# Kernel optimization log

Hardware: AMD Instinct MI355X
Metric: run time of the kernel (lower is better)

The kernel has to match this reference:

```python
import jax, jax.numpy as jnp
import numpy as np

D_MODEL = 1024
N_HEADS = 16
HEAD_DIM = D_MODEL // N_HEADS
D_FF = 4096
EPS = 1e-5


def setup_inputs() -> dict:
    key = jax.random.key(0)
    ks = jax.random.split(key, 12)
    s = 0.02
    return {
        "x": jax.random.normal(ks[0], (2, 2048, D_MODEL), jnp.float32),
        "wq": jax.random.normal(ks[1], (D_MODEL, D_MODEL), jnp.float32) * s,
        "bq": jnp.zeros((D_MODEL,), jnp.float32),
        "wk": jax.random.normal(ks[2], (D_MODEL, D_MODEL), jnp.float32) * s,
        "bk": jnp.zeros((D_MODEL,), jnp.float32),
        "wv": jax.random.normal(ks[3], (D_MODEL, D_MODEL), jnp.float32) * s,
        "bv": jnp.zeros((D_MODEL,), jnp.float32),
        "wo": jax.random.normal(ks[4], (D_MODEL, D_MODEL), jnp.float32) * s,
        "bo": jnp.zeros((D_MODEL,), jnp.float32),
        "w1": jax.random.normal(ks[5], (D_MODEL, D_FF), jnp.float32) * s,
        "b1": jnp.zeros((D_FF,), jnp.float32),
        "w2": jax.random.normal(ks[6], (D_FF, D_MODEL), jnp.float32) * s,
        "b2": jnp.zeros((D_MODEL,), jnp.float32),
        "g1": jnp.ones((D_MODEL,), jnp.float32),
        "be1": jnp.zeros((D_MODEL,), jnp.float32),
        "g2": jnp.ones((D_MODEL,), jnp.float32),
        "be2": jnp.zeros((D_MODEL,), jnp.float32),
    }


def _layer_norm(x, g, b):
    mu = jnp.mean(x, axis=-1, keepdims=True)
    var = jnp.var(x, axis=-1, keepdims=True)
    return (x - mu) * jax.lax.rsqrt(var + EPS) * g + b


def reference(x, wq, bq, wk, bk, wv, bv, wo, bo, w1, b1, w2, b2, g1, be1, g2, be2):
    B, S, D = x.shape
    nx = _layer_norm(x, g1, be1)
    # projections -> [B, H, S, d]
    def split_heads(t):
        return t.reshape(B, S, N_HEADS, HEAD_DIM).transpose(0, 2, 1, 3)
    q = split_heads(nx @ wq + bq)
    k = split_heads(nx @ wk + bk)
    v = split_heads(nx @ wv + bv)
    scores = jnp.einsum("bhqd,bhkd->bhqk", q, k) / jnp.sqrt(jnp.float32(HEAD_DIM))
    attn = jax.nn.softmax(scores, axis=-1)
    out = jnp.einsum("bhqk,bhkd->bhqd", attn, v)
    out = out.transpose(0, 2, 1, 3).reshape(B, S, D)
    x = x + (out @ wo + bo)
    nx = _layer_norm(x, g2, be2)
    ff = jax.nn.relu(nx @ w1 + b1) @ w2 + b2
    return x + ff
```

## Files before the change

### kernel.cpp

```cpp
#include <hip/hip_runtime.h>


typedef __attribute__((ext_vector_type(8))) unsigned short u16x8;
typedef __attribute__((ext_vector_type(4))) unsigned short u16x4;
typedef __attribute__((ext_vector_type(8))) __bf16 bf16x8;
typedef __attribute__((ext_vector_type(4))) float f32x4;
typedef __attribute__((ext_vector_type(4))) unsigned int u32x4;

#define C_SCALE 0.1803368801111f

static __device__ __forceinline__ unsigned short f2b(float f) {
    return __builtin_bit_cast(unsigned short, (__bf16)f);
}
static __device__ __forceinline__ float b2f(unsigned short h) {
    unsigned u = ((unsigned)h) << 16;
    float f;
    __builtin_memcpy(&f, &u, 4);
    return f;
}

static __device__ __forceinline__ void async_cp16(
    const unsigned short* g, unsigned short* l)
{
    __builtin_amdgcn_global_load_lds(
        (const __attribute__((address_space(1))) unsigned int*)g,
        (__attribute__((address_space(3))) unsigned int*)l,
        16, 0, 0);
}

__global__ __launch_bounds__(256) void transpose_all_k(
    const float* __restrict__ wq, const float* __restrict__ wk,
    const float* __restrict__ wv, const float* __restrict__ wo,
    const float* __restrict__ w1, const float* __restrict__ w2,
    unsigned short* __restrict__ wqkvT, unsigned short* __restrict__ woT,
    unsigned short* __restrict__ w1T, unsigned short* __restrict__ w2T)
{
    __shared__ unsigned short tile[32][33];
    const int ti = blockIdx.x;
    const float* in;
    unsigned short* out;
    int R, C, bi, bj;
    float sc = 1.0f;
    if (ti < 4096) {
        R = 1024; C = 1024;
        bi = (ti & 1023) >> 5; bj = ti & 31;
        int z = ti >> 10;
        in = (z == 0) ? wq : (z == 1) ? wk : (z == 2) ? wv : wo;
        out = (z < 3) ? wqkvT + (size_t)z * 1024 * 1024 : woT;
        if (z == 1) sc = C_SCALE;
    } else if (ti < 8192) {
        R = 1024; C = 4096;
        int l = ti - 4096;
        bi = l >> 7; bj = l & 127;
        in = w1; out = w1T;
    } else {
        R = 4096; C = 1024;
        int l = ti - 8192;
        bi = l >> 5; bj = l & 31;
        in = w2; out = w2T;
    }
    const int tx = threadIdx.x & 31, ty = threadIdx.x >> 5;
#pragma unroll
    for (int rr = 0; rr < 4; ++rr) {
        int r = ty + rr * 8;
        tile[r][tx] = f2b(in[(size_t)(bi * 32 + r) * C + bj * 32 + tx] * sc);
    }
    __syncthreads();
#pragma unroll
    for (int rr = 0; rr < 4; ++rr) {
        int r = ty + rr * 8;
        out[(size_t)(bj * 32 + r) * R + bi * 32 + tx] = tile[tx][r];
    }
}

__global__ __launch_bounds__(256) void concat3_k(
    const float* __restrict__ a, const float* __restrict__ b,
    const float* __restrict__ c, float* __restrict__ o)
{
    int t = blockIdx.x * 256 + threadIdx.x;
    float v = (t < 1024) ? a[t]
            : ((t < 2048) ? b[t - 1024] * C_SCALE : c[t - 2048]);
    o[t] = v;
}

__global__ __launch_bounds__(256) void ln_kernel(
    const float* __restrict__ x, const float* __restrict__ g,
    const float* __restrict__ be, unsigned short* __restrict__ o)
{
    const int row = blockIdx.x;
    const int t = threadIdx.x;
    const float* xr = x + (size_t)row * 1024;
    float4 v4 = *reinterpret_cast<const float4*>(&xr[t * 4]);
    float f[4] = {v4.x, v4.y, v4.z, v4.w};
    float s = f[0] + f[1] + f[2] + f[3];
    float ss = f[0] * f[0] + f[1] * f[1] + f[2] * f[2] + f[3] * f[3];
#pragma unroll
    for (int d = 1; d < 64; d <<= 1) {
        s += __shfl_xor(s, d);
        ss += __shfl_xor(ss, d);
    }
    __shared__ float sb[4], ssb[4];
    const int wave = t >> 6;
    if ((t & 63) == 0) { sb[wave] = s; ssb[wave] = ss; }
    __syncthreads();
    s = sb[0] + sb[1] + sb[2] + sb[3];
    ss = ssb[0] + ssb[1] + ssb[2] + ssb[3];
    const float mu = s * (1.0f / 1024.0f);
    const float var = ss * (1.0f / 1024.0f) - mu * mu;
    const float rs = rsqrtf(var + 1e-5f);
    u16x4 r4;
#pragma unroll
    for (int j = 0; j < 4; ++j)
        r4[j] = f2b((f[j] - mu) * rs * g[t * 4 + j] + be[t * 4 + j]);
    *reinterpret_cast<u16x4*>(&o[(size_t)row * 1024 + t * 4]) = r4;
}

__global__ __launch_bounds__(256) void reduce_ln_kernel(
    const unsigned short* __restrict__ pa, const unsigned short* __restrict__ pb,
    const float* __restrict__ bias, const float* __restrict__ x,
    const float* __restrict__ g, const float* __restrict__ be,
    float* __restrict__ x2, unsigned short* __restrict__ o)
{
    const int row = blockIdx.x;
    const int t = threadIdx.x;
    const size_t base = (size_t)row * 1024 + t * 4;
    float4 x4 = *reinterpret_cast<const float4*>(&x[base]);
    float4 bb = *reinterpret_cast<const float4*>(&bias[t * 4]);
    float f[4] = {x4.x + bb.x, x4.y + bb.y, x4.z + bb.z, x4.w + bb.w};
#pragma unroll
    for (int z = 0; z < 2; ++z) {
        u16x4 va = *reinterpret_cast<const u16x4*>(&pa[(size_t)z * 4096 * 1024 + base]);
        u16x4 vb = *reinterpret_cast<const u16x4*>(&pb[(size_t)z * 4096 * 1024 + base]);
#pragma unroll
        for (int j = 0; j < 4; ++j) f[j] += b2f(va[j]) + b2f(vb[j]);
    }
    *reinterpret_cast<float4*>(&x2[base]) = {f[0], f[1], f[2], f[3]};
    float s = f[0] + f[1] + f[2] + f[3];
    float ss = f[0] * f[0] + f[1] * f[1] + f[2] * f[2] + f[3] * f[3];
#pragma unroll
    for (int d = 1; d < 64; d <<= 1) {
        s += __shfl_xor(s, d);
        ss += __shfl_xor(ss, d);
    }
    __shared__ float sb[4], ssb[4];
    const int wave = t >> 6;
    if ((t & 63) == 0) { sb[wave] = s; ssb[wave] = ss; }
    __syncthreads();
    s = sb[0] + sb[1] + sb[2] + sb[3];
    ss = ssb[0] + ssb[1] + ssb[2] + ssb[3];
    const float mu = s * (1.0f / 1024.0f);
    const float var = ss * (1.0f / 1024.0f) - mu * mu;
    const float rs = rsqrtf(var + 1e-5f);
    u16x4 r4;
#pragma unroll
    for (int j = 0; j < 4; ++j)
        r4[j] = f2b((f[j] - mu) * rs * g[t * 4 + j] + be[t * 4 + j]);
    *reinterpret_cast<u16x4*>(&o[base]) = r4;
}

__global__ __launch_bounds__(256) void reduce_out4_k(
    const unsigned short* __restrict__ pa, const unsigned short* __restrict__ pb,
    const float* __restrict__ bias, const float* __restrict__ x2,
    float* __restrict__ out)
{
    const size_t i4 = ((size_t)blockIdx.x * 256 + threadIdx.x) * 4;
    float4 x4 = *reinterpret_cast<const float4*>(&x2[i4]);
    float4 bb = *reinterpret_cast<const float4*>(&bias[i4 & 1023]);
    float a0 = x4.x + bb.x, a1 = x4.y + bb.y, a2 = x4.z + bb.z, a3 = x4.w + bb.w;
#pragma unroll
    for (int z = 0; z < 2; ++z) {
        u16x4 va = *reinterpret_cast<const u16x4*>(&pa[(size_t)z * 4096 * 1024 + i4]);
        u16x4 vb = *reinterpret_cast<const u16x4*>(&pb[(size_t)z * 4096 * 1024 + i4]);
        a0 += b2f(va[0]) + b2f(vb[0]);
        a1 += b2f(va[1]) + b2f(vb[1]);
        a2 += b2f(va[2]) + b2f(vb[2]);
        a3 += b2f(va[3]) + b2f(vb[3]);
    }
    *reinterpret_cast<float4*>(&out[i4]) = {a0, a1, a2, a3};
}

template<int MODE, int RELU>
__global__ __launch_bounds__(256, 4) void gemm_bt(
    const unsigned short* __restrict__ A, int lda,
    const unsigned short* __restrict__ Bt, int ldb,
    const float* __restrict__ bias,
    void* __restrict__ Cv, void* __restrict__ Cv2, int N, int Kloop)
{
    __shared__ unsigned short As[128 * 32];
    __shared__ unsigned short Bs[128 * 32];
    const int t = threadIdx.x;
    const int wave = t >> 6, lane = t & 63;
    const int quad = lane >> 4, l16 = lane & 15;
    const int wm = wave >> 1, wn = wave & 1;
    const int m0 = blockIdx.y * 128;
    const int n0 = blockIdx.x * 128;
    const int k0 = blockIdx.z * Kloop;
    const int rl = lane >> 2;
    const int cl = (lane & 3) * 8;

    f32x4 acc[4][4];
#pragma unroll
    for (int mi = 0; mi < 4; ++mi)
#pragma unroll
        for (int ni = 0; ni < 4; ++ni) acc[mi][ni] = {0.f, 0.f, 0.f, 0.f};

    for (int kt = 0; kt < Kloop; kt += 32) {
#pragma unroll
        for (int j = 0; j < 4; ++j) {
            int c = wave * 4 + j;
            if (c < 8) {
                async_cp16(&A[(size_t)(m0 + c * 16 + rl) * lda + k0 + kt + cl],
                           &As[c * 512 + lane * 8]);
            } else {
                int bc = c - 8;
                async_cp16(&Bt[(size_t)(n0 + bc * 16 + rl) * ldb + k0 + kt + cl],
                           &Bs[bc * 512 + lane * 8]);
            }
        }
        __syncthreads();
        bf16x8 af[4], bfr[4];
#pragma unroll
        for (int mi = 0; mi < 4; ++mi)
            af[mi] = __builtin_bit_cast(bf16x8,
                *reinterpret_cast<const u16x8*>(&As[(wm * 64 + mi * 16 + l16) * 32 + quad * 8]));
#pragma unroll
        for (int ni = 0; ni < 4; ++ni)
            bfr[ni] = __builtin_bit_cast(bf16x8,
                *reinterpret_cast<const u16x8*>(&Bs[(wn * 64 + ni * 16 + l16) * 32 + quad * 8]));
#pragma unroll
        for (int mi = 0; mi < 4; ++mi)
#pragma unroll
            for (int ni = 0; ni < 4; ++ni)
                acc[mi][ni] = __builtin_amdgcn_mfma_f32_16x16x32_bf16(
                    af[mi], bfr[ni], acc[mi][ni], 0, 0, 0);
        __syncthreads();
    }

#pragma unroll
    for (int mi = 0; mi < 4; ++mi) {
        const int gr0 = m0 + wm * 64 + mi * 16 + quad * 4;
#pragma unroll
        for (int ni = 0; ni < 4; ++ni) {
            const int gc = n0 + wn * 64 + ni * 16 + l16;
            if (MODE == 2) {
                const float bv = bias[gc];
                if (gc < 2048) {
#pragma unroll
                    for (int r = 0; r < 4; ++r)
                        ((unsigned short*)Cv)[(size_t)(gr0 + r) * 2048 + gc] =
                            f2b(acc[mi][ni][r] + bv);
                } else {
                    u16x4 pk;
#pragma unroll
                    for (int r = 0; r < 4; ++r) pk[r] = f2b(acc[mi][ni][r] + bv);
                    const int b = gr0 >> 11, s0 = gr0 & 2047;
                    *reinterpret_cast<u16x4*>(
                        &((unsigned short*)Cv2)[((size_t)b * 1024 + (gc - 2048)) * 2048 + s0]) = pk;
                }
            } else if (MODE == 5) {
                unsigned short* base = (blockIdx.z < 2)
                    ? (unsigned short*)Cv  + (size_t)blockIdx.z * 4096 * N
                    : (unsigned short*)Cv2 + (size_t)(blockIdx.z - 2) * 4096 * N;
#pragma unroll
                for (int r = 0; r < 4; ++r)
                    base[(size_t)(gr0 + r) * N + gc] = f2b(acc[mi][ni][r]);
            } else {
                const float bv = bias[gc];
#pragma unroll
                for (int r = 0; r < 4; ++r) {
                    float v = acc[mi][ni][r] + bv;
                    if (RELU) v = fmaxf(v, 0.f);
                    ((unsigned short*)Cv)[(size_t)(gr0 + r) * N + gc] = f2b(v);
                }
            }
        }
    }
}

__global__ __launch_bounds__(256, 2) void attn_kernel(
    const unsigned short* __restrict__ qkb, const unsigned short* __restrict__ vbT,
    unsigned short* __restrict__ ao)
{
    __shared__ unsigned short Ks[2][64][72];
    __shared__ unsigned short Vt[2][64][72];
    const int t = threadIdx.x;
    const int lane = t & 63;
    const int quad = lane >> 4, l16 = lane & 15;
    const int wave = t >> 6;
    const int bh = blockIdx.y;
    const int b = bh >> 4, h = bh & 15;
    const int q0 = blockIdx.x * 128 + wave * 32;
    const size_t qk_base = (size_t)b * 2048 * 2048;
    const size_t vt_base = (size_t)b * 1024 * 2048 + (size_t)h * 64 * 2048;

    bf16x8 qf[2][2];
#pragma unroll
    for (int m = 0; m < 2; ++m)
#pragma unroll
        for (int kk = 0; kk < 2; ++kk)
            qf[m][kk] = __builtin_bit_cast(bf16x8, *reinterpret_cast<const u16x8*>(
                &qkb[qk_base + (size_t)(q0 + m * 16 + l16) * 2048 + h * 64 + kk * 32 + quad * 8]));

    u16x8 ones_u;
#pragma unroll
    for (int j = 0; j < 8; ++j) ones_u[j] = 0x3F80;
    const bf16x8 onesf = __builtin_bit_cast(bf16x8, ones_u);

    f32x4 o_acc[2][4], l_frag[2];
#pragma unroll
    for (int m = 0; m < 2; ++m) {
        l_frag[m] = {0.f, 0.f, 0.f, 0.f};
#pragma unroll
        for (int nf = 0; nf < 4; ++nf) o_acc[m][nf] = {0.f, 0.f, 0.f, 0.f};
    }

    const int srow0 = t >> 3, sc8 = (t & 7) * 8;
    const int srow1 = srow0 + 32;

    const unsigned short* kg0 = &qkb[qk_base + (size_t)srow0 * 2048 + 1024 + h * 64 + sc8];
    const unsigned short* kg1 = kg0 + (size_t)32 * 2048;
    const unsigned short* vg0 = &vbT[vt_base + (size_t)srow0 * 2048 + sc8];
    const unsigned short* vg1 = vg0 + (size_t)32 * 2048;

    u16x8 kr[2], vr[2];
    kr[0] = *reinterpret_cast<const u16x8*>(kg0);
    kr[1] = *reinterpret_cast<const u16x8*>(kg1);
    vr[0] = *reinterpret_cast<const u16x8*>(vg0);
    vr[1] = *reinterpret_cast<const u16x8*>(vg1);
    *reinterpret_cast<u16x8*>(&Ks[0][srow0][sc8]) = kr[0];
    *reinterpret_cast<u16x8*>(&Ks[0][srow1][sc8]) = kr[1];
    *reinterpret_cast<u16x8*>(&Vt[0][srow0][sc8]) = vr[0];
    *reinterpret_cast<u16x8*>(&Vt[0][srow1][sc8]) = vr[1];
    kr[0] = *reinterpret_cast<const u16x8*>(kg0 + (size_t)64 * 2048);
    kr[1] = *reinterpret_cast<const u16x8*>(kg1 + (size_t)64 * 2048);
    vr[0] = *reinterpret_cast<const u16x8*>(vg0 + 64);
    vr[1] = *reinterpret_cast<const u16x8*>(vg1 + 64);
    __syncthreads();

    for (int it = 0; it < 32; ++it) {
        const int cur = it & 1, nxt = cur ^ 1;
        if (it + 1 < 32) {
            *reinterpret_cast<u16x8*>(&Ks[nxt][srow0][sc8]) = kr[0];
            *reinterpret_cast<u16x8*>(&Ks[nxt][srow1][sc8]) = kr[1];
            *reinterpret_cast<u16x8*>(&Vt[nxt][srow0][sc8]) = vr[0];
            *reinterpret_cast<u16x8*>(&Vt[nxt][srow1][sc8]) = vr[1];
        }
        if (it + 2 < 32) {
            const size_t ko = (size_t)(it + 2) * 64 * 2048;
            const int vo = (it + 2) * 64;
            kr[0] = *reinterpret_cast<const u16x8*>(kg0 + ko);
            kr[1] = *reinterpret_cast<const u16x8*>(kg1 + ko);
            vr[0] = *reinterpret_cast<const u16x8*>(vg0 + vo);
            vr[1] = *reinterpret_cast<const u16x8*>(vg1 + vo);
        }

#pragma unroll
        for (int kh = 0; kh < 2; ++kh) {
            unsigned d0[2][2], d1[2][2];
#pragma unroll
            for (int kfi = 0; kfi < 2; ++kfi) {
                const int kf = kh * 2 + kfi;
                bf16x8 kfr0 = __builtin_bit_cast(bf16x8,
                    *reinterpret_cast<const u16x8*>(&Ks[cur][kf * 16 + l16][quad * 8]));
                bf16x8 kfr1 = __builtin_bit_cast(bf16x8,
                    *reinterpret_cast<const u16x8*>(&Ks[cur][kf * 16 + l16][32 + quad * 8]));
#pragma unroll
                for (int m = 0; m < 2; ++m) {
                    f32x4 s = {0.f, 0.f, 0.f, 0.f};
                    s = __builtin_amdgcn_mfma_f32_16x16x32_bf16(kfr0, qf[m][0], s, 0, 0, 0);
                    s = __builtin_amdgcn_mfma_f32_16x16x32_bf16(kfr1, qf[m][1], s, 0, 0, 0);
                    d0[m][kfi] = (unsigned)f2b(exp2f(s[0])) |
                                 ((unsigned)f2b(exp2f(s[1])) << 16);
                    d1[m][kfi] = (unsigned)f2b(exp2f(s[2])) |
                                 ((unsigned)f2b(exp2f(s[3])) << 16);
                }
            }
            bf16x8 pfr[2];
#pragma unroll
            for (int m = 0; m < 2; ++m) {
                unsigned x0 = d0[m][0], y0 = d0[m][1];
                unsigned x1 = d1[m][0], y1 = d1[m][1];
                asm("v_permlane32_swap_b32 %0, %1\n\t"
                    "v_permlane16_swap_b32 %0, %1"
                    : "+v"(x0), "+v"(y0));
                asm("v_permlane32_swap_b32 %0, %1\n\t"
                    "v_permlane16_swap_b32 %0, %1"
                    : "+v"(x1), "+v"(y1));
                u32x4 pw = {x0, x1, y0, y1};
                pfr[m] = __builtin_bit_cast(bf16x8, pw);
                l_frag[m] = __builtin_amdgcn_mfma_f32_16x16x32_bf16(
                    pfr[m], onesf, l_frag[m], 0, 0, 0);
            }
#pragma unroll
            for (int nf = 0; nf < 4; ++nf) {
                bf16x8 vfr = __builtin_bit_cast(bf16x8,
                    *reinterpret_cast<const u16x8*>(&Vt[cur][nf * 16 + l16][kh * 32 + quad * 8]));
#pragma unroll
                for (int m = 0; m < 2; ++m)
                    o_acc[m][nf] = __builtin_amdgcn_mfma_f32_16x16x32_bf16(
                        pfr[m], vfr, o_acc[m][nf], 0, 0, 0);
            }
        }
        __syncthreads();
    }

#pragma unroll
    for (int m = 0; m < 2; ++m) {
#pragma unroll
        for (int r = 0; r < 4; ++r) {
            const float inv = 1.0f / l_frag[m][r];
            const int row = q0 + m * 16 + quad * 4 + r;
#pragma unroll
            for (int nf = 0; nf < 4; ++nf)
                ao[(size_t)b * 2048 * 1024 + (size_t)row * 1024 + h * 64 + nf * 16 + l16] =
                    f2b(o_acc[m][nf][r] * inv);
        }
    }
}

extern "C" void kernel_launch(void* const* d_in, const int* in_sizes, int n_in,
                              void* d_out, int out_size, void* d_ws, size_t ws_size,
                              hipStream_t stream)
{
    const float* x   = (const float*)d_in[0];
    const float* wq  = (const float*)d_in[1];
    const float* bq  = (const float*)d_in[2];
    const float* wk  = (const float*)d_in[3];
    const float* bk  = (const float*)d_in[4];
    const float* wv  = (const float*)d_in[5];
    const float* bv  = (const float*)d_in[6];
    const float* wo  = (const float*)d_in[7];
    const float* bo  = (const float*)d_in[8];
    const float* w1  = (const float*)d_in[9];
    const float* b1  = (const float*)d_in[10];
    const float* w2  = (const float*)d_in[11];
    const float* b2  = (const float*)d_in[12];
    const float* g1  = (const float*)d_in[13];
    const float* be1 = (const float*)d_in[14];
    const float* g2  = (const float*)d_in[15];
    const float* be2 = (const float*)d_in[16];
    float* out = (float*)d_out;
    char*  ws  = (char*)d_ws;

    const int M = 4096, D = 1024, DFF = 4096;
    const size_t MB = 1 << 20;

    unsigned short* wqkvT = (unsigned short*)(ws + 0 * MB);
    unsigned short* woT   = (unsigned short*)(ws + 6 * MB);
    unsigned short* w1T   = (unsigned short*)(ws + 8 * MB);
    unsigned short* w2T   = (unsigned short*)(ws + 16 * MB);
    unsigned short* ln    = (unsigned short*)(ws + 24 * MB);
    unsigned short* qkb   = (unsigned short*)(ws + 32 * MB);
    unsigned short* vbT   = (unsigned short*)(ws + 48 * MB);
    unsigned short* ao    = (unsigned short*)(ws + 56 * MB);
    unsigned short* ff1   = (unsigned short*)(ws + 32 * MB);
    float*          x2    = (float*)(ws + 64 * MB);
    float*          bqkv  = (float*)(ws + 80 * MB);
    unsigned short* pHi   = (unsigned short*)(ws + 80 * MB);
    unsigned short* pOlo  = (unsigned short*)(ws + 32 * MB);
    unsigned short* pFlo  = (unsigned short*)(ws + 0 * MB);

    transpose_all_k<<<12288, 256, 0, stream>>>(wq, wk, wv, wo, w1, w2,
                                               wqkvT, woT, w1T, w2T);
    concat3_k<<<12, 256, 0, stream>>>(bq, bk, bv, bqkv);
    ln_kernel<<<M, 256, 0, stream>>>(x, g1, be1, ln);
    gemm_bt<2, 0><<<dim3(24, 32), 256, 0, stream>>>(
        ln, D, wqkvT, D, bqkv, qkb, vbT, 3072, D);
    attn_kernel<<<dim3(16, 32), 256, 0, stream>>>(qkb, vbT, ao);
    gemm_bt<5, 0><<<dim3(8, 32, 4), 256, 0, stream>>>(
        ao, D, woT, D, nullptr, pHi, pOlo, 1024, 256);
    reduce_ln_kernel<<<M, 256, 0, stream>>>(pHi, pOlo, bo, x, g2, be2, x2, ln);
    gemm_bt<0, 1><<<dim3(32, 32), 256, 0, stream>>>(
        ln, D, w1T, D, b1, ff1, nullptr, DFF, D);
    gemm_bt<5, 0><<<dim3(8, 32, 4), 256, 0, stream>>>(
        ff1, DFF, w2T, DFF, nullptr, pHi, pFlo, 1024, 1024);
    reduce_out4_k<<<4096, 256, 0, stream>>>(pHi, pFlo, b2, x2, out);
}
```

Baseline: 381.2 us.

## Halve attention query tile per wave and raise occupancy with more blocks

```diff
diff --git a/kernel.cpp b/kernel.cpp
--- a/kernel.cpp
+++ b/kernel.cpp
@@ -277,7 +277,7 @@
     }
 }
 
-__global__ __launch_bounds__(256, 2) void attn_kernel(
+__global__ __launch_bounds__(256, 4) void attn_kernel(
     const unsigned short* __restrict__ qkb, const unsigned short* __restrict__ vbT,
     unsigned short* __restrict__ ao)
 {
@@ -289,30 +289,25 @@
     const int wave = t >> 6;
     const int bh = blockIdx.y;
     const int b = bh >> 4, h = bh & 15;
-    const int q0 = blockIdx.x * 128 + wave * 32;
+    const int q0 = blockIdx.x * 64 + wave * 16;
     const size_t qk_base = (size_t)b * 2048 * 2048;
     const size_t vt_base = (size_t)b * 1024 * 2048 + (size_t)h * 64 * 2048;
 
-    bf16x8 qf[2][2];
-#pragma unroll
-    for (int m = 0; m < 2; ++m)
-#pragma unroll
-        for (int kk = 0; kk < 2; ++kk)
-            qf[m][kk] = __builtin_bit_cast(bf16x8, *reinterpret_cast<const u16x8*>(
-                &qkb[qk_base + (size_t)(q0 + m * 16 + l16) * 2048 + h * 64 + kk * 32 + quad * 8]));
+    bf16x8 qf[2];
+#pragma unroll
+    for (int kk = 0; kk < 2; ++kk)
+        qf[kk] = __builtin_bit_cast(bf16x8, *reinterpret_cast<const u16x8*>(
+            &qkb[qk_base + (size_t)(q0 + l16) * 2048 + h * 64 + kk * 32 + quad * 8]));
 
     u16x8 ones_u;
 #pragma unroll
     for (int j = 0; j < 8; ++j) ones_u[j] = 0x3F80;
     const bf16x8 onesf = __builtin_bit_cast(bf16x8, ones_u);
 
-    f32x4 o_acc[2][4], l_frag[2];
-#pragma unroll
-    for (int m = 0; m < 2; ++m) {
-        l_frag[m] = {0.f, 0.f, 0.f, 0.f};
-#pragma unroll
-        for (int nf = 0; nf < 4; ++nf) o_acc[m][nf] = {0.f, 0.f, 0.f, 0.f};
-    }
+    f32x4 o_acc[4], l_frag;
+    l_frag = {0.f, 0.f, 0.f, 0.f};
+#pragma unroll
+    for (int nf = 0; nf < 4; ++nf) o_acc[nf] = {0.f, 0.f, 0.f, 0.f};
 
     const int srow0 = t >> 3, sc8 = (t & 7) * 8;
     const int srow1 = srow0 + 32;
@@ -356,7 +351,7 @@
 
 #pragma unroll
         for (int kh = 0; kh < 2; ++kh) {
-            unsigned d0[2][2], d1[2][2];
+            unsigned d0[2], d1[2];
 #pragma unroll
             for (int kfi = 0; kfi < 2; ++kfi) {
                 const int kf = kh * 2 + kfi;
@@ -364,57 +359,47 @@
                     *reinterpret_cast<const u16x8*>(&Ks[cur][kf * 16 + l16][quad * 8]));
                 bf16x8 kfr1 = __builtin_bit_cast(bf16x8,
                     *reinterpret_cast<const u16x8*>(&Ks[cur][kf * 16 + l16][32 + quad * 8]));
-#pragma unroll
-                for (int m = 0; m < 2; ++m) {
-                    f32x4 s = {0.f, 0.f, 0.f, 0.f};
-                    s = __builtin_amdgcn_mfma_f32_16x16x32_bf16(kfr0, qf[m][0], s, 0, 0, 0);
-                    s = __builtin_amdgcn_mfma_f32_16x16x32_bf16(kfr1, qf[m][1], s, 0, 0, 0);
-                    d0[m][kfi] = (unsigned)f2b(exp2f(s[0])) |
-                                 ((unsigned)f2b(exp2f(s[1])) << 16);
-                    d1[m][kfi] = (unsigned)f2b(exp2f(s[2])) |
-                                 ((unsigned)f2b(exp2f(s[3])) << 16);
-                }
+                f32x4 s = {0.f, 0.f, 0.f, 0.f};
+                s = __builtin_amdgcn_mfma_f32_16x16x32_bf16(kfr0, qf[0], s, 0, 0, 0);
+                s = __builtin_amdgcn_mfma_f32_16x16x32_bf16(kfr1, qf[1], s, 0, 0, 0);
+                d0[kfi] = (unsigned)f2b(exp2f(s[0])) |
+                          ((unsigned)f2b(exp2f(s[1])) << 16);
+                d1[kfi] = (unsigned)f2b(exp2f(s[2])) |
+                          ((unsigned)f2b(exp2f(s[3])) << 16);
             }
-            bf16x8 pfr[2];
-#pragma unroll
-            for (int m = 0; m < 2; ++m) {
-                unsigned x0 = d0[m][0], y0 = d0[m][1];
-                unsigned x1 = d1[m][0], y1 = d1[m][1];
-                asm("v_permlane32_swap_b32 %0, %1\n\t"
-                    "v_permlane16_swap_b32 %0, %1"
-                    : "+v"(x0), "+v"(y0));
-                asm("v_permlane32_swap_b32 %0, %1\n\t"
-                    "v_permlane16_swap_b32 %0, %1"
-                    : "+v"(x1), "+v"(y1));
-                u32x4 pw = {x0, x1, y0, y1};
-                pfr[m] = __builtin_bit_cast(bf16x8, pw);
-                l_frag[m] = __builtin_amdgcn_mfma_f32_16x16x32_bf16(
-                    pfr[m], onesf, l_frag[m], 0, 0, 0);
-            }
+            unsigned x0 = d0[0], y0 = d0[1];
+            unsigned x1 = d1[0], y1 = d1[1];
+            asm("v_permlane32_swap_b32 %0, %1\n\t"
+                "v_permlane16_swap_b32 %0, %1"
+                : "+v"(x0), "+v"(y0));
+            asm("v_permlane32_swap_b32 %0, %1\n\t"
+                "v_permlane16_swap_b32 %0, %1"
+                : "+v"(x1), "+v"(y1));
+            u32x4 pw = {x0, x1, y0, y1};
+            bf16x8 pfr = __builtin_bit_cast(bf16x8, pw);
+            l_frag = __builtin_amdgcn_mfma_f32_16x16x32_bf16(
+                pfr, onesf, l_frag, 0, 0, 0);
+            __builtin_amdgcn_s_setprio(1);
 #pragma unroll
             for (int nf = 0; nf < 4; ++nf) {
                 bf16x8 vfr = __builtin_bit_cast(bf16x8,
                     *reinterpret_cast<const u16x8*>(&Vt[cur][nf * 16 + l16][kh * 32 + quad * 8]));
-#pragma unroll
-                for (int m = 0; m < 2; ++m)
-                    o_acc[m][nf] = __builtin_amdgcn_mfma_f32_16x16x32_bf16(
-                        pfr[m], vfr, o_acc[m][nf], 0, 0, 0);
+                o_acc[nf] = __builtin_amdgcn_mfma_f32_16x16x32_bf16(
+                    pfr, vfr, o_acc[nf], 0, 0, 0);
             }
+            __builtin_amdgcn_s_setprio(0);
         }
         __syncthreads();
     }
 
 #pragma unroll
-    for (int m = 0; m < 2; ++m) {
-#pragma unroll
-        for (int r = 0; r < 4; ++r) {
-            const float inv = 1.0f / l_frag[m][r];
-            const int row = q0 + m * 16 + quad * 4 + r;
-#pragma unroll
-            for (int nf = 0; nf < 4; ++nf)
-                ao[(size_t)b * 2048 * 1024 + (size_t)row * 1024 + h * 64 + nf * 16 + l16] =
-                    f2b(o_acc[m][nf][r] * inv);
-        }
+    for (int r = 0; r < 4; ++r) {
+        const float inv = 1.0f / l_frag[r];
+        const int row = q0 + quad * 4 + r;
+#pragma unroll
+        for (int nf = 0; nf < 4; ++nf)
+            ao[(size_t)b * 2048 * 1024 + (size_t)row * 1024 + h * 64 + nf * 16 + l16] =
+                f2b(o_acc[nf][r] * inv);
     }
 }
 
@@ -466,7 +451,7 @@
     ln_kernel<<<M, 256, 0, stream>>>(x, g1, be1, ln);
     gemm_bt<2, 0><<<dim3(24, 32), 256, 0, stream>>>(
         ln, D, wqkvT, D, bqkv, qkb, vbT, 3072, D);
-    attn_kernel<<<dim3(16, 32), 256, 0, stream>>>(qkb, vbT, ao);
+    attn_kernel<<<dim3(32, 32), 256, 0, stream>>>(qkb, vbT, ao);
     gemm_bt<5, 0><<<dim3(8, 32, 4), 256, 0, stream>>>(
         ao, D, woT, D, nullptr, pHi, pOlo, 1024, 256);
     reduce_ln_kernel<<<M, 256, 0, stream>>>(pHi, pOlo, bo, x, g2, be2, x2, ln);
```

Result: no change. 378.9 us (-0.6%).

## Load attention K/V fragments directly from global into registers, dropping LDS staging

Applied to the files above, without the earlier changes.

```diff
diff --git a/kernel.cpp b/kernel.cpp
--- a/kernel.cpp
+++ b/kernel.cpp
@@ -281,8 +281,6 @@
     const unsigned short* __restrict__ qkb, const unsigned short* __restrict__ vbT,
     unsigned short* __restrict__ ao)
 {
-    __shared__ unsigned short Ks[2][64][72];
-    __shared__ unsigned short Vt[2][64][72];
     const int t = threadIdx.x;
     const int lane = t & 63;
     const int quad = lane >> 4, l16 = lane & 15;
@@ -314,72 +312,50 @@
         for (int nf = 0; nf < 4; ++nf) o_acc[m][nf] = {0.f, 0.f, 0.f, 0.f};
     }
 
-    const int srow0 = t >> 3, sc8 = (t & 7) * 8;
-    const int srow1 = srow0 + 32;
-
-    const unsigned short* kg0 = &qkb[qk_base + (size_t)srow0 * 2048 + 1024 + h * 64 + sc8];
-    const unsigned short* kg1 = kg0 + (size_t)32 * 2048;
-    const unsigned short* vg0 = &vbT[vt_base + (size_t)srow0 * 2048 + sc8];
-    const unsigned short* vg1 = vg0 + (size_t)32 * 2048;
-
-    u16x8 kr[2], vr[2];
-    kr[0] = *reinterpret_cast<const u16x8*>(kg0);
-    kr[1] = *reinterpret_cast<const u16x8*>(kg1);
-    vr[0] = *reinterpret_cast<const u16x8*>(vg0);
-    vr[1] = *reinterpret_cast<const u16x8*>(vg1);
-    *reinterpret_cast<u16x8*>(&Ks[0][srow0][sc8]) = kr[0];
-    *reinterpret_cast<u16x8*>(&Ks[0][srow1][sc8]) = kr[1];
-    *reinterpret_cast<u16x8*>(&Vt[0][srow0][sc8]) = vr[0];
-    *reinterpret_cast<u16x8*>(&Vt[0][srow1][sc8]) = vr[1];
-    kr[0] = *reinterpret_cast<const u16x8*>(kg0 + (size_t)64 * 2048);
-    kr[1] = *reinterpret_cast<const u16x8*>(kg1 + (size_t)64 * 2048);
-    vr[0] = *reinterpret_cast<const u16x8*>(vg0 + 64);
-    vr[1] = *reinterpret_cast<const u16x8*>(vg1 + 64);
-    __syncthreads();
-
-    for (int it = 0; it < 32; ++it) {
-        const int cur = it & 1, nxt = cur ^ 1;
-        if (it + 1 < 32) {
-            *reinterpret_cast<u16x8*>(&Ks[nxt][srow0][sc8]) = kr[0];
-            *reinterpret_cast<u16x8*>(&Ks[nxt][srow1][sc8]) = kr[1];
-            *reinterpret_cast<u16x8*>(&Vt[nxt][srow0][sc8]) = vr[0];
-            *reinterpret_cast<u16x8*>(&Vt[nxt][srow1][sc8]) = vr[1];
-        }
-        if (it + 2 < 32) {
-            const size_t ko = (size_t)(it + 2) * 64 * 2048;
-            const int vo = (it + 2) * 64;
-            kr[0] = *reinterpret_cast<const u16x8*>(kg0 + ko);
-            kr[1] = *reinterpret_cast<const u16x8*>(kg1 + ko);
-            vr[0] = *reinterpret_cast<const u16x8*>(vg0 + vo);
-            vr[1] = *reinterpret_cast<const u16x8*>(vg1 + vo);
-        }
-
+    const unsigned short* kp[4];
+    const unsigned short* vp[4];
+#pragma unroll
+    for (int f = 0; f < 4; ++f) {
+        kp[f] = &qkb[qk_base + (size_t)(f * 16 + l16) * 2048 + 1024 + h * 64 + quad * 8];
+        vp[f] = &vbT[vt_base + (size_t)(f * 16 + l16) * 2048 + quad * 8];
+    }
+
+    auto load_tile = [&](u16x8 (&nk)[8], u16x8 (&nv)[8]) {
+#pragma unroll
+        for (int f = 0; f < 4; ++f) {
+            nk[f * 2 + 0] = *reinterpret_cast<const u16x8*>(kp[f]);
+            nk[f * 2 + 1] = *reinterpret_cast<const u16x8*>(kp[f] + 32);
+            nv[f * 2 + 0] = *reinterpret_cast<const u16x8*>(vp[f]);
+            nv[f * 2 + 1] = *reinterpret_cast<const u16x8*>(vp[f] + 32);
+            kp[f] += (size_t)64 * 2048;
+            vp[f] += 64;
+        }
+    };
+
+    auto compute = [&](u16x8 (&ck)[8], u16x8 (&cv)[8]) {
+        unsigned d0[2][4], d1[2][4];
+#pragma unroll
+        for (int kf = 0; kf < 4; ++kf) {
+            bf16x8 kfr0 = __builtin_bit_cast(bf16x8, ck[kf * 2 + 0]);
+            bf16x8 kfr1 = __builtin_bit_cast(bf16x8, ck[kf * 2 + 1]);
+#pragma unroll
+            for (int m = 0; m < 2; ++m) {
+                f32x4 s = {0.f, 0.f, 0.f, 0.f};
+                s = __builtin_amdgcn_mfma_f32_16x16x32_bf16(kfr0, qf[m][0], s, 0, 0, 0);
+                s = __builtin_amdgcn_mfma_f32_16x16x32_bf16(kfr1, qf[m][1], s, 0, 0, 0);
+                d0[m][kf] = (unsigned)f2b(exp2f(s[0])) |
+                            ((unsigned)f2b(exp2f(s[1])) << 16);
+                d1[m][kf] = (unsigned)f2b(exp2f(s[2])) |
+                            ((unsigned)f2b(exp2f(s[3])) << 16);
+            }
+        }
 #pragma unroll
         for (int kh = 0; kh < 2; ++kh) {
-            unsigned d0[2][2], d1[2][2];
-#pragma unroll
-            for (int kfi = 0; kfi < 2; ++kfi) {
-                const int kf = kh * 2 + kfi;
-                bf16x8 kfr0 = __builtin_bit_cast(bf16x8,
-                    *reinterpret_cast<const u16x8*>(&Ks[cur][kf * 16 + l16][quad * 8]));
-                bf16x8 kfr1 = __builtin_bit_cast(bf16x8,
-                    *reinterpret_cast<const u16x8*>(&Ks[cur][kf * 16 + l16][32 + quad * 8]));
-#pragma unroll
-                for (int m = 0; m < 2; ++m) {
-                    f32x4 s = {0.f, 0.f, 0.f, 0.f};
-                    s = __builtin_amdgcn_mfma_f32_16x16x32_bf16(kfr0, qf[m][0], s, 0, 0, 0);
-                    s = __builtin_amdgcn_mfma_f32_16x16x32_bf16(kfr1, qf[m][1], s, 0, 0, 0);
-                    d0[m][kfi] = (unsigned)f2b(exp2f(s[0])) |
-                                 ((unsigned)f2b(exp2f(s[1])) << 16);
-                    d1[m][kfi] = (unsigned)f2b(exp2f(s[2])) |
-                                 ((unsigned)f2b(exp2f(s[3])) << 16);
-                }
-            }
             bf16x8 pfr[2];
 #pragma unroll
             for (int m = 0; m < 2; ++m) {
-                unsigned x0 = d0[m][0], y0 = d0[m][1];
-                unsigned x1 = d1[m][0], y1 = d1[m][1];
+                unsigned x0 = d0[m][kh * 2], y0 = d0[m][kh * 2 + 1];
+                unsigned x1 = d1[m][kh * 2], y1 = d1[m][kh * 2 + 1];
                 asm("v_permlane32_swap_b32 %0, %1\n\t"
                     "v_permlane16_swap_b32 %0, %1"
                     : "+v"(x0), "+v"(y0));
@@ -391,17 +367,26 @@
                 l_frag[m] = __builtin_amdgcn_mfma_f32_16x16x32_bf16(
                     pfr[m], onesf, l_frag[m], 0, 0, 0);
             }
+            __builtin_amdgcn_s_setprio(1);
 #pragma unroll
             for (int nf = 0; nf < 4; ++nf) {
-                bf16x8 vfr = __builtin_bit_cast(bf16x8,
-                    *reinterpret_cast<const u16x8*>(&Vt[cur][nf * 16 + l16][kh * 32 + quad * 8]));
+                bf16x8 vfr = __builtin_bit_cast(bf16x8, cv[nf * 2 + kh]);
 #pragma unroll
                 for (int m = 0; m < 2; ++m)
                     o_acc[m][nf] = __builtin_amdgcn_mfma_f32_16x16x32_bf16(
                         pfr[m], vfr, o_acc[m][nf], 0, 0, 0);
             }
-        }
-        __syncthreads();
+            __builtin_amdgcn_s_setprio(0);
+        }
+    };
+
+    u16x8 kA[8], vA[8], kB[8], vB[8];
+    load_tile(kA, vA);
+    for (int it2 = 0; it2 < 16; ++it2) {
+        load_tile(kB, vB);
+        compute(kA, vA);
+        if (it2 < 15) load_tile(kA, vA);
+        compute(kB, vB);
     }
 
 #pragma unroll
```

After: 436.6 us. +14.5%, slower.
